# Kernel tuning notes

Measured on AMD Instinct MI355X. Metric: run time of the kernel, lower is better.

Reference implementation:

```python
import jax, jax.numpy as jnp
import numpy as np

HIDDEN = 4096
N_EXPERTS = 128
TOP_K = 8
N_GROUP = 1
TOPK_GROUP = 1
ROUTED_SCALING = 1.0
NORM_TOPK_PROB = True


def setup_inputs() -> dict:
    key = jax.random.key(0)
    k1, k2 = jax.random.split(key)
    tokens = 16384  # batch 4 * seq 4096
    hidden_states = jax.random.normal(k1, (tokens, HIDDEN), dtype=jnp.float32)
    # router gate weight (n_routed_experts, hidden_size)
    weight = jax.random.normal(k2, (N_EXPERTS, HIDDEN), dtype=jnp.float32) * 0.02
    # e_score_correction_bias buffer, initialized to zeros in the module
    e_score_correction_bias = jnp.zeros((N_EXPERTS,), dtype=jnp.float32)
    return {"hidden_states": hidden_states, "weight": weight,
            "e_score_correction_bias": e_score_correction_bias}


def _get_topk_indices(scores, bias):
    # scores: [T, E] sigmoid gate scores; bias: [E]
    T = scores.shape[0]
    experts_per_group = N_EXPERTS // N_GROUP
    s = scores + bias[None, :]  # scores_for_choice
    # group score: sum of top-2 corrected scores within each group
    grp = s.reshape(T, N_GROUP, experts_per_group)
    group_scores = jnp.sum(jax.lax.top_k(grp, 2)[0], axis=-1)  # [T, G]
    group_idx = jax.lax.top_k(group_scores, TOPK_GROUP)[1]      # [T, topk_group]
    group_mask = jnp.zeros((T, N_GROUP), dtype=bool).at[
        jnp.arange(T)[:, None], group_idx].set(True)
    score_mask = jnp.repeat(group_mask, experts_per_group, axis=-1)  # [T, E]
    s_masked = jnp.where(score_mask, s, 0.0)
    topk_indices = jax.lax.top_k(s_masked, TOP_K)[1]  # [T, top_k]
    return topk_indices


def reference(hidden_states, weight, e_score_correction_bias):
    x = hidden_states.reshape(-1, HIDDEN).astype(jnp.float32)
    router_logits = x @ weight.astype(jnp.float32).T          # [T, E]
    scores = jax.nn.sigmoid(router_logits)
    topk_indices = _get_topk_indices(scores, e_score_correction_bias)
    topk_weights = jnp.take_along_axis(scores, topk_indices, axis=1)  # [T, top_k]
    if NORM_TOPK_PROB:
        denom = jnp.sum(topk_weights, axis=-1, keepdims=True) + 1e-20
        topk_weights = topk_weights / denom
    topk_weights = topk_weights * ROUTED_SCALING
    return topk_indices, topk_weights
```

## Files before the change

### kernel.cpp

```cpp
#include <hip/hip_runtime.h>
#include <math.h>

#define HIDDEN 4096
#define NEXP   128
#define TOPK   8
#define BT     32
#define CHUNK  64
#define NCHUNK (HIDDEN / CHUNK)
#define SSTR   132
#define PLANE  (NEXP * CHUNK)

typedef int v4i __attribute__((ext_vector_type(4)));

static __device__ __forceinline__ unsigned pack4(int a, int b, int c, int d) {
    return (unsigned)(a & 255) | ((unsigned)(b & 255) << 8) |
           ((unsigned)(c & 255) << 16) | ((unsigned)(d & 255) << 24);
}

static __device__ __forceinline__ void slice5(float val, float scale1,
        int& d0, int& d1, int& d2, int& d3, int& d4) {
    float v = val * scale1;
    float f = __builtin_rintf(v);
    float r = v - f;
    int nh = (int)f;
    int nl = (int)__builtin_rintf(r * 2097152.0f);
    d0 = (nh + 64) >> 7;  d1 = nh - (d0 << 7);
    d2 = (nl + 8192) >> 14;
    int r2 = nl - (d2 << 14);
    d3 = (r2 + 64) >> 7;  d4 = r2 - (d3 << 7);
}

static __device__ __forceinline__ void slice4(float val, float scale1,
        int& d0, int& d1, int& d2, int& d3) {
    float v = val * scale1;
    float f = __builtin_rintf(v);
    float r = v - f;
    int nh = (int)f;
    int nl = (int)__builtin_rintf(r * 16384.0f);
    d0 = (nh + 64) >> 7;  d1 = nh - (d0 << 7);
    d2 = (nl + 64) >> 7;  d3 = nl - (d2 << 7);
}

__global__ __launch_bounds__(256)
void slice_w_kernel(const float* __restrict__ W, signed char* __restrict__ P)
{
    const int t  = blockIdx.x * 256 + threadIdx.x;
    const int e  = t >> 9;
    const int k0 = (t & 511) * 8;
    const float* src = W + (size_t)e * HIDDEN + k0;
    const float4 a = ((const float4*)src)[0];
    const float4 b = ((const float4*)src)[1];

    int p00,p01,p02,p03,p04; slice5(a.x, 32768.0f, p00,p01,p02,p03,p04);
    int p10,p11,p12,p13,p14; slice5(a.y, 32768.0f, p10,p11,p12,p13,p14);
    int p20,p21,p22,p23,p24; slice5(a.z, 32768.0f, p20,p21,p22,p23,p24);
    int p30,p31,p32,p33,p34; slice5(a.w, 32768.0f, p30,p31,p32,p33,p34);
    int p40,p41,p42,p43,p44; slice5(b.x, 32768.0f, p40,p41,p42,p43,p44);
    int p50,p51,p52,p53,p54; slice5(b.y, 32768.0f, p50,p51,p52,p53,p54);
    int p60,p61,p62,p63,p64; slice5(b.z, 32768.0f, p60,p61,p62,p63,p64);
    int p70,p71,p72,p73,p74; slice5(b.w, 32768.0f, p70,p71,p72,p73,p74);

    const int c = k0 >> 6, kin = k0 & 63;
    signed char* base = P + ((size_t)(c * 5) * NEXP + e) * CHUNK + kin;
    uint2 v;
    v.x = pack4(p00,p10,p20,p30); v.y = pack4(p40,p50,p60,p70);
    *(uint2*)(base + 0 * PLANE) = v;
    v.x = pack4(p01,p11,p21,p31); v.y = pack4(p41,p51,p61,p71);
    *(uint2*)(base + 1 * PLANE) = v;
    v.x = pack4(p02,p12,p22,p32); v.y = pack4(p42,p52,p62,p72);
    *(uint2*)(base + 2 * PLANE) = v;
    v.x = pack4(p03,p13,p23,p33); v.y = pack4(p43,p53,p63,p73);
    *(uint2*)(base + 3 * PLANE) = v;
    v.x = pack4(p04,p14,p24,p34); v.y = pack4(p44,p54,p64,p74);
    *(uint2*)(base + 4 * PLANE) = v;
}

static __device__ __forceinline__ void slice_pack16(
        const float4 f0, const float4 f1, const float4 f2, const float4 f3,
        v4i& s0, v4i& s1, v4i& s2, v4i& s3)
{
    unsigned w0[4], w1[4], w2[4], w3[4];
    {
        int a0,b0,c0,d0, a1,b1,c1,d1, a2,b2,c2,d2, a3,b3,c3,d3;
        slice4(f0.x, 1024.0f, a0,a1,a2,a3);
        slice4(f0.y, 1024.0f, b0,b1,b2,b3);
        slice4(f0.z, 1024.0f, c0,c1,c2,c3);
        slice4(f0.w, 1024.0f, d0,d1,d2,d3);
        w0[0] = pack4(a0,b0,c0,d0); w1[0] = pack4(a1,b1,c1,d1);
        w2[0] = pack4(a2,b2,c2,d2); w3[0] = pack4(a3,b3,c3,d3);
    }
    {
        int a0,b0,c0,d0, a1,b1,c1,d1, a2,b2,c2,d2, a3,b3,c3,d3;
        slice4(f1.x, 1024.0f, a0,a1,a2,a3);
        slice4(f1.y, 1024.0f, b0,b1,b2,b3);
        slice4(f1.z, 1024.0f, c0,c1,c2,c3);
        slice4(f1.w, 1024.0f, d0,d1,d2,d3);
        w0[1] = pack4(a0,b0,c0,d0); w1[1] = pack4(a1,b1,c1,d1);
        w2[1] = pack4(a2,b2,c2,d2); w3[1] = pack4(a3,b3,c3,d3);
    }
    {
        int a0,b0,c0,d0, a1,b1,c1,d1, a2,b2,c2,d2, a3,b3,c3,d3;
        slice4(f2.x, 1024.0f, a0,a1,a2,a3);
        slice4(f2.y, 1024.0f, b0,b1,b2,b3);
        slice4(f2.z, 1024.0f, c0,c1,c2,c3);
        slice4(f2.w, 1024.0f, d0,d1,d2,d3);
        w0[2] = pack4(a0,b0,c0,d0); w1[2] = pack4(a1,b1,c1,d1);
        w2[2] = pack4(a2,b2,c2,d2); w3[2] = pack4(a3,b3,c3,d3);
    }
    {
        int a0,b0,c0,d0, a1,b1,c1,d1, a2,b2,c2,d2, a3,b3,c3,d3;
        slice4(f3.x, 1024.0f, a0,a1,a2,a3);
        slice4(f3.y, 1024.0f, b0,b1,b2,b3);
        slice4(f3.z, 1024.0f, c0,c1,c2,c3);
        slice4(f3.w, 1024.0f, d0,d1,d2,d3);
        w0[3] = pack4(a0,b0,c0,d0); w1[3] = pack4(a1,b1,c1,d1);
        w2[3] = pack4(a2,b2,c2,d2); w3[3] = pack4(a3,b3,c3,d3);
    }
    s0 = (v4i){(int)w0[0], (int)w0[1], (int)w0[2], (int)w0[3]};
    s1 = (v4i){(int)w1[0], (int)w1[1], (int)w1[2], (int)w1[3]};
    s2 = (v4i){(int)w2[0], (int)w2[1], (int)w2[2], (int)w2[3]};
    s3 = (v4i){(int)w3[0], (int)w3[1], (int)w3[2], (int)w3[3]};
}

__global__ __launch_bounds__(256, 2)
void router_kernel(const float* __restrict__ X,
                   const signed char* __restrict__ P,
                   const float* __restrict__ Bias,
                   float* __restrict__ Out, int T)
{
    __shared__ double S[BT * SSTR];

    const int tid  = threadIdx.x;
    const int lane = tid & 63;
    const int wave = tid >> 6;
    const int tokBase = blockIdx.x * BT;

    const int m = lane & 15;
    const int q = lane >> 4;

    int r0 = tokBase + m;      if (r0 >= T) r0 = T - 1;
    int r1 = tokBase + 16 + m; if (r1 >= T) r1 = T - 1;
    const float* xp0 = X + (size_t)r0 * HIDDEN + q * 16;
    const float* xp1 = X + (size_t)r1 * HIDDEN + q * 16;

    const int eb0 = wave * 32 + m;
    const size_t boff0 = (size_t)eb0 * CHUNK + q * 16;
    const size_t boff1 = boff0 + (size_t)16 * CHUNK;

    v4i acc[2][2][5];
    #pragma unroll
    for (int tt = 0; tt < 2; tt++)
        #pragma unroll
        for (int et = 0; et < 2; et++)
            #pragma unroll
            for (int s = 0; s < 5; s++)
                acc[tt][et][s] = (v4i){0, 0, 0, 0};

    #pragma unroll 2
    for (int c = 0; c < NCHUNK; c++) {
        const float4* x0 = (const float4*)(xp0 + c * CHUNK);
        const float4* x1 = (const float4*)(xp1 + c * CHUNK);
        const float4 f00 = x0[0], f01 = x0[1], f02 = x0[2], f03 = x0[3];
        const float4 f10 = x1[0], f11 = x1[1], f12 = x1[2], f13 = x1[3];

        const signed char* pc = P + (size_t)(c * 5) * PLANE;
        v4i b0[5], b1[5];
        #pragma unroll
        for (int s = 0; s < 5; s++) {
            b0[s] = *(const v4i*)(pc + (size_t)s * PLANE + boff0);
            b1[s] = *(const v4i*)(pc + (size_t)s * PLANE + boff1);
        }

        v4i a0[4], a1[4];
        slice_pack16(f00, f01, f02, f03, a0[0], a0[1], a0[2], a0[3]);
        slice_pack16(f10, f11, f12, f13, a1[0], a1[1], a1[2], a1[3]);

        #pragma unroll
        for (int tt = 0; tt < 2; tt++) {
            const v4i A0 = tt ? a1[0] : a0[0];
            const v4i A1 = tt ? a1[1] : a0[1];
            const v4i A2 = tt ? a1[2] : a0[2];
            const v4i A3 = tt ? a1[3] : a0[3];
            #pragma unroll
            for (int et = 0; et < 2; et++) {
                const v4i B0 = et ? b1[0] : b0[0];
                const v4i B1 = et ? b1[1] : b0[1];
                const v4i B2 = et ? b1[2] : b0[2];
                const v4i B3 = et ? b1[3] : b0[3];
                const v4i B4 = et ? b1[4] : b0[4];
                acc[tt][et][0] = __builtin_amdgcn_mfma_i32_16x16x64_i8(A0, B0, acc[tt][et][0], 0, 0, 0);
                acc[tt][et][1] = __builtin_amdgcn_mfma_i32_16x16x64_i8(A0, B1, acc[tt][et][1], 0, 0, 0);
                acc[tt][et][1] = __builtin_amdgcn_mfma_i32_16x16x64_i8(A1, B0, acc[tt][et][1], 0, 0, 0);
                acc[tt][et][2] = __builtin_amdgcn_mfma_i32_16x16x64_i8(A0, B2, acc[tt][et][2], 0, 0, 0);
                acc[tt][et][2] = __builtin_amdgcn_mfma_i32_16x16x64_i8(A1, B1, acc[tt][et][2], 0, 0, 0);
                acc[tt][et][2] = __builtin_amdgcn_mfma_i32_16x16x64_i8(A2, B0, acc[tt][et][2], 0, 0, 0);
                acc[tt][et][3] = __builtin_amdgcn_mfma_i32_16x16x64_i8(A0, B3, acc[tt][et][3], 0, 0, 0);
                acc[tt][et][3] = __builtin_amdgcn_mfma_i32_16x16x64_i8(A1, B2, acc[tt][et][3], 0, 0, 0);
                acc[tt][et][3] = __builtin_amdgcn_mfma_i32_16x16x64_i8(A2, B1, acc[tt][et][3], 0, 0, 0);
                acc[tt][et][3] = __builtin_amdgcn_mfma_i32_16x16x64_i8(A3, B0, acc[tt][et][3], 0, 0, 0);
                acc[tt][et][4] = __builtin_amdgcn_mfma_i32_16x16x64_i8(A0, B4, acc[tt][et][4], 0, 0, 0);
                acc[tt][et][4] = __builtin_amdgcn_mfma_i32_16x16x64_i8(A1, B3, acc[tt][et][4], 0, 0, 0);
                acc[tt][et][4] = __builtin_amdgcn_mfma_i32_16x16x64_i8(A2, B2, acc[tt][et][4], 0, 0, 0);
                acc[tt][et][4] = __builtin_amdgcn_mfma_i32_16x16x64_i8(A3, B1, acc[tt][et][4], 0, 0, 0);
            }
        }
    }

    {
        const double w0 = 0x1p-11, w1 = 0x1p-18, w2 = 0x1p-25, w3 = 0x1p-32, w4 = 0x1p-39;
        #pragma unroll
        for (int tt = 0; tt < 2; tt++)
            #pragma unroll
            for (int et = 0; et < 2; et++) {
                const int ecol = wave * 32 + et * 16 + m;
                const double bias = (double)Bias[ecol];
                #pragma unroll
                for (int r = 0; r < 4; r++) {
                    const int trow = tt * 16 + q * 4 + r;
                    const double logit = (double)acc[tt][et][0][r] * w0
                                       + (double)acc[tt][et][1][r] * w1
                                       + (double)acc[tt][et][2][r] * w2
                                       + (double)acc[tt][et][3][r] * w3
                                       + (double)acc[tt][et][4][r] * w4;
                    S[trow * SSTR + ecol] = 1.0 / (1.0 + exp(-logit)) + bias;
                }
            }
    }
    __syncthreads();

    {
        const int tk  = tid >> 3;
        const int j   = tid & 7;
        const int tok = tokBase + tk;
        const double* row = S + tk * SSTR + j * 16;
        double v[16];
        #pragma unroll
        for (int k = 0; k < 16; k++) v[k] = row[k];

        double wts[TOPK]; float idxf[TOPK];
        double wsum = 0.0;
        #pragma unroll
        for (int p = 0; p < TOPK; p++) {
            double best = v[0]; int bi = 0;
            #pragma unroll
            for (int k = 1; k < 16; k++)
                if (v[k] > best) { best = v[k]; bi = k; }
            int be = j * 16 + bi;
            #pragma unroll
            for (int off = 1; off < 8; off <<= 1) {
                double ob = __shfl_xor(best, off, 8);
                int    oe = __shfl_xor(be,   off, 8);
                if (ob > best || (ob == best && oe < be)) { best = ob; be = oe; }
            }
            const bool own = (be >> 4) == j;
            const int  bl  = be & 15;
            #pragma unroll
            for (int k = 0; k < 16; k++)
                if (own && k == bl) v[k] = -1.0e300;
            const double sg = best - (double)Bias[be];
            wts[p]  = sg;
            wsum   += sg;
            idxf[p] = (float)be;
        }
        if (j == 0 && tok < T) {
            const double inv = 1.0 / (wsum + 1e-20);
            float* oi = Out + (size_t)tok * TOPK;
            float* ow = Out + (size_t)T * TOPK + (size_t)tok * TOPK;
            #pragma unroll
            for (int p = 0; p < TOPK; p++) {
                oi[p] = idxf[p];
                ow[p] = (float)(wts[p] * inv);
            }
        }
    }
}

extern "C" void kernel_launch(void* const* d_in, const int* in_sizes, int n_in,
                              void* d_out, int out_size, void* d_ws, size_t ws_size,
                              hipStream_t stream) {
    const float* X    = (const float*)d_in[0];
    const float* W    = (const float*)d_in[1];
    const float* Bias = (const float*)d_in[2];
    float* Out = (float*)d_out;
    const int T = in_sizes[0] / HIDDEN;
    signed char* P = (signed char*)d_ws;

    hipLaunchKernelGGL(slice_w_kernel, dim3(NEXP * 512 / 256), dim3(256), 0, stream, W, P);
    hipLaunchKernelGGL(router_kernel, dim3((T + BT - 1) / BT), dim3(256), 0, stream,
                       X, P, Bias, Out, T);
}
```

Measured before the change: 508.5 us.

## Double token tile per block, prefetch activations, drop lowest-order slice products

Each block now handles 64 tokens, with each wave covering 32 tokens by 64 experts, so every loaded weight fragment feeds more MFMAs. Activation loads are software-pipelined two chunks ahead, and slicing runs one chunk ahead of the MFMAs. The lowest-significance weight slice (plane 4) is no longer loaded or multiplied, which cuts MFMA and load work but reduces the precision of the emulated fp32 logits. Launch bounds move to one block per SM to make room for the larger accumulator set, and the top-k phase uses 4 threads per token instead of 8.

```diff
diff --git a/kernel.cpp b/kernel.cpp
--- a/kernel.cpp
+++ b/kernel.cpp
@@ -4,7 +4,7 @@
 #define HIDDEN 4096
 #define NEXP   128
 #define TOPK   8
-#define BT     32
+#define BT     64
 #define CHUNK  64
 #define NCHUNK (HIDDEN / CHUNK)
 #define SSTR   132
@@ -122,7 +122,7 @@
     s3 = (v4i){(int)w3[0], (int)w3[1], (int)w3[2], (int)w3[3]};
 }
 
-__global__ __launch_bounds__(256, 2)
+__global__ __launch_bounds__(256, 1)
 void router_kernel(const float* __restrict__ X,
                    const signed char* __restrict__ P,
                    const float* __restrict__ Bias,
@@ -137,57 +137,76 @@
 
     const int m = lane & 15;
     const int q = lane >> 4;
-
-    int r0 = tokBase + m;      if (r0 >= T) r0 = T - 1;
-    int r1 = tokBase + 16 + m; if (r1 >= T) r1 = T - 1;
+    const int tpair = wave & 1;
+    const int ehalf = wave >> 1;
+
+    int r0 = tokBase + tpair * 32 + m;      if (r0 >= T) r0 = T - 1;
+    int r1 = tokBase + tpair * 32 + 16 + m; if (r1 >= T) r1 = T - 1;
     const float* xp0 = X + (size_t)r0 * HIDDEN + q * 16;
     const float* xp1 = X + (size_t)r1 * HIDDEN + q * 16;
 
-    const int eb0 = wave * 32 + m;
-    const size_t boff0 = (size_t)eb0 * CHUNK + q * 16;
-    const size_t boff1 = boff0 + (size_t)16 * CHUNK;
-
-    v4i acc[2][2][5];
+    const size_t boffBase = (size_t)(ehalf * 64 + m) * CHUNK + (size_t)q * 16;
+
+    v4i acc[2][4][5];
     #pragma unroll
     for (int tt = 0; tt < 2; tt++)
         #pragma unroll
-        for (int et = 0; et < 2; et++)
+        for (int et = 0; et < 4; et++)
             #pragma unroll
             for (int s = 0; s < 5; s++)
                 acc[tt][et][s] = (v4i){0, 0, 0, 0};
 
-    #pragma unroll 2
+    v4i aC[2][4];
+    float4 xn[8];
+    {
+        const float4* x0 = (const float4*)xp0;
+        const float4* x1 = (const float4*)xp1;
+        const float4 c0 = x0[0], c1 = x0[1], c2 = x0[2], c3 = x0[3];
+        const float4 c4 = x1[0], c5 = x1[1], c6 = x1[2], c7 = x1[3];
+        slice_pack16(c0, c1, c2, c3, aC[0][0], aC[0][1], aC[0][2], aC[0][3]);
+        slice_pack16(c4, c5, c6, c7, aC[1][0], aC[1][1], aC[1][2], aC[1][3]);
+        const float4* y0 = (const float4*)(xp0 + CHUNK);
+        const float4* y1 = (const float4*)(xp1 + CHUNK);
+        xn[0] = y0[0]; xn[1] = y0[1]; xn[2] = y0[2]; xn[3] = y0[3];
+        xn[4] = y1[0]; xn[5] = y1[1]; xn[6] = y1[2]; xn[7] = y1[3];
+    }
+
+    #pragma unroll 1
     for (int c = 0; c < NCHUNK; c++) {
-        const float4* x0 = (const float4*)(xp0 + c * CHUNK);
-        const float4* x1 = (const float4*)(xp1 + c * CHUNK);
-        const float4 f00 = x0[0], f01 = x0[1], f02 = x0[2], f03 = x0[3];
-        const float4 f10 = x1[0], f11 = x1[1], f12 = x1[2], f13 = x1[3];
-
         const signed char* pc = P + (size_t)(c * 5) * PLANE;
-        v4i b0[5], b1[5];
-        #pragma unroll
-        for (int s = 0; s < 5; s++) {
-            b0[s] = *(const v4i*)(pc + (size_t)s * PLANE + boff0);
-            b1[s] = *(const v4i*)(pc + (size_t)s * PLANE + boff1);
+        v4i B[4][4];
+        #pragma unroll
+        for (int et = 0; et < 4; et++)
+            #pragma unroll
+            for (int s = 0; s < 4; s++)
+                B[et][s] = *(const v4i*)(pc + (size_t)s * PLANE + boffBase
+                                            + (size_t)(et * 16) * CHUNK);
+
+        float4 x2[8];
+        {
+            const int cn = (c + 2) & (NCHUNK - 1);
+            const float4* y0 = (const float4*)(xp0 + cn * CHUNK);
+            const float4* y1 = (const float4*)(xp1 + cn * CHUNK);
+            x2[0] = y0[0]; x2[1] = y0[1]; x2[2] = y0[2]; x2[3] = y0[3];
+            x2[4] = y1[0]; x2[5] = y1[1]; x2[6] = y1[2]; x2[7] = y1[3];
         }
 
-        v4i a0[4], a1[4];
-        slice_pack16(f00, f01, f02, f03, a0[0], a0[1], a0[2], a0[3]);
-        slice_pack16(f10, f11, f12, f13, a1[0], a1[1], a1[2], a1[3]);
+        v4i aN[2][4];
+        slice_pack16(xn[0], xn[1], xn[2], xn[3], aN[0][0], aN[0][1], aN[0][2], aN[0][3]);
+        slice_pack16(xn[4], xn[5], xn[6], xn[7], aN[1][0], aN[1][1], aN[1][2], aN[1][3]);
 
         #pragma unroll
         for (int tt = 0; tt < 2; tt++) {
-            const v4i A0 = tt ? a1[0] : a0[0];
-            const v4i A1 = tt ? a1[1] : a0[1];
-            const v4i A2 = tt ? a1[2] : a0[2];
-            const v4i A3 = tt ? a1[3] : a0[3];
-            #pragma unroll
-            for (int et = 0; et < 2; et++) {
-                const v4i B0 = et ? b1[0] : b0[0];
-                const v4i B1 = et ? b1[1] : b0[1];
-                const v4i B2 = et ? b1[2] : b0[2];
-                const v4i B3 = et ? b1[3] : b0[3];
-                const v4i B4 = et ? b1[4] : b0[4];
+            const v4i A0 = aC[tt][0];
+            const v4i A1 = aC[tt][1];
+            const v4i A2 = aC[tt][2];
+            const v4i A3 = aC[tt][3];
+            #pragma unroll
+            for (int et = 0; et < 4; et++) {
+                const v4i B0 = B[et][0];
+                const v4i B1 = B[et][1];
+                const v4i B2 = B[et][2];
+                const v4i B3 = B[et][3];
                 acc[tt][et][0] = __builtin_amdgcn_mfma_i32_16x16x64_i8(A0, B0, acc[tt][et][0], 0, 0, 0);
                 acc[tt][et][1] = __builtin_amdgcn_mfma_i32_16x16x64_i8(A0, B1, acc[tt][et][1], 0, 0, 0);
                 acc[tt][et][1] = __builtin_amdgcn_mfma_i32_16x16x64_i8(A1, B0, acc[tt][et][1], 0, 0, 0);
@@ -198,12 +217,20 @@
                 acc[tt][et][3] = __builtin_amdgcn_mfma_i32_16x16x64_i8(A1, B2, acc[tt][et][3], 0, 0, 0);
                 acc[tt][et][3] = __builtin_amdgcn_mfma_i32_16x16x64_i8(A2, B1, acc[tt][et][3], 0, 0, 0);
                 acc[tt][et][3] = __builtin_amdgcn_mfma_i32_16x16x64_i8(A3, B0, acc[tt][et][3], 0, 0, 0);
-                acc[tt][et][4] = __builtin_amdgcn_mfma_i32_16x16x64_i8(A0, B4, acc[tt][et][4], 0, 0, 0);
                 acc[tt][et][4] = __builtin_amdgcn_mfma_i32_16x16x64_i8(A1, B3, acc[tt][et][4], 0, 0, 0);
                 acc[tt][et][4] = __builtin_amdgcn_mfma_i32_16x16x64_i8(A2, B2, acc[tt][et][4], 0, 0, 0);
                 acc[tt][et][4] = __builtin_amdgcn_mfma_i32_16x16x64_i8(A3, B1, acc[tt][et][4], 0, 0, 0);
             }
         }
+
+        #pragma unroll
+        for (int i = 0; i < 2; i++)
+            #pragma unroll
+            for (int s = 0; s < 4; s++)
+                aC[i][s] = aN[i][s];
+        #pragma unroll
+        for (int i = 0; i < 8; i++)
+            xn[i] = x2[i];
     }
 
     {
@@ -211,12 +238,12 @@
         #pragma unroll
         for (int tt = 0; tt < 2; tt++)
             #pragma unroll
-            for (int et = 0; et < 2; et++) {
-                const int ecol = wave * 32 + et * 16 + m;
+            for (int et = 0; et < 4; et++) {
+                const int ecol = ehalf * 64 + et * 16 + m;
                 const double bias = (double)Bias[ecol];
                 #pragma unroll
                 for (int r = 0; r < 4; r++) {
-                    const int trow = tt * 16 + q * 4 + r;
+                    const int trow = tpair * 32 + tt * 16 + q * 4 + r;
                     const double logit = (double)acc[tt][et][0][r] * w0
                                        + (double)acc[tt][et][1][r] * w1
                                        + (double)acc[tt][et][2][r] * w2
@@ -229,13 +256,13 @@
     __syncthreads();
 
     {
-        const int tk  = tid >> 3;
-        const int j   = tid & 7;
+        const int tk  = tid >> 2;
+        const int j   = tid & 3;
         const int tok = tokBase + tk;
-        const double* row = S + tk * SSTR + j * 16;
-        double v[16];
-        #pragma unroll
-        for (int k = 0; k < 16; k++) v[k] = row[k];
+        const double* row = S + tk * SSTR + j * 32;
+        double v[32];
+        #pragma unroll
+        for (int k = 0; k < 32; k++) v[k] = row[k];
 
         double wts[TOPK]; float idxf[TOPK];
         double wsum = 0.0;
@@ -243,19 +270,19 @@
         for (int p = 0; p < TOPK; p++) {
             double best = v[0]; int bi = 0;
             #pragma unroll
-            for (int k = 1; k < 16; k++)
+            for (int k = 1; k < 32; k++)
                 if (v[k] > best) { best = v[k]; bi = k; }
-            int be = j * 16 + bi;
-            #pragma unroll
-            for (int off = 1; off < 8; off <<= 1) {
-                double ob = __shfl_xor(best, off, 8);
-                int    oe = __shfl_xor(be,   off, 8);
+            int be = j * 32 + bi;
+            #pragma unroll
+            for (int off = 1; off < 4; off <<= 1) {
+                double ob = __shfl_xor(best, off, 4);
+                int    oe = __shfl_xor(be,   off, 4);
                 if (ob > best || (ob == best && oe < be)) { best = ob; be = oe; }
             }
-            const bool own = (be >> 4) == j;
-            const int  bl  = be & 15;
-            #pragma unroll
-            for (int k = 0; k < 16; k++)
+            const bool own = (be >> 5) == j;
+            const int  bl  = be & 31;
+            #pragma unroll
+            for (int k = 0; k < 32; k++)
                 if (own && k == bl) v[k] = -1.0e300;
             const double sg = best - (double)Bias[be];
             wts[p]  = sg;
```

Result: slower. 685.1 us (+34.7%).

## Double-buffer chunk loads, widen block to 64 tokens, drop lowest slice product

Applied to the files above, without the earlier changes.

The router kernel becomes a software-pipelined loop: while the MFMAs for the current chunk run, the next chunk's X values and int8 weight slices are loaded into separate even and odd register buffers. Blocks grow to 512 threads and 64 tokens, and the waves are split across token halves and expert quarters. The sliced product now uses 13 MFMAs instead of 14 and loads 4 weight planes instead of 5, dropping the A0*B4 term. That removes work but slightly lowers logit precision, and the larger block uses more registers and LDS.

```diff
diff --git a/kernel.cpp b/kernel.cpp
--- a/kernel.cpp
+++ b/kernel.cpp
@@ -4,7 +4,7 @@
 #define HIDDEN 4096
 #define NEXP   128
 #define TOPK   8
-#define BT     32
+#define BT     64
 #define CHUNK  64
 #define NCHUNK (HIDDEN / CHUNK)
 #define SSTR   132
@@ -122,7 +122,22 @@
     s3 = (v4i){(int)w3[0], (int)w3[1], (int)w3[2], (int)w3[3]};
 }
 
-__global__ __launch_bounds__(256, 2)
+#define PYR13(A0, A1, A2, A3, BF, ACC)                                         \
+    ACC[0] = __builtin_amdgcn_mfma_i32_16x16x64_i8(A0, BF[0], ACC[0], 0, 0, 0); \
+    ACC[1] = __builtin_amdgcn_mfma_i32_16x16x64_i8(A0, BF[1], ACC[1], 0, 0, 0); \
+    ACC[2] = __builtin_amdgcn_mfma_i32_16x16x64_i8(A0, BF[2], ACC[2], 0, 0, 0); \
+    ACC[3] = __builtin_amdgcn_mfma_i32_16x16x64_i8(A0, BF[3], ACC[3], 0, 0, 0); \
+    ACC[4] = __builtin_amdgcn_mfma_i32_16x16x64_i8(A1, BF[3], ACC[4], 0, 0, 0); \
+    ACC[1] = __builtin_amdgcn_mfma_i32_16x16x64_i8(A1, BF[0], ACC[1], 0, 0, 0); \
+    ACC[2] = __builtin_amdgcn_mfma_i32_16x16x64_i8(A1, BF[1], ACC[2], 0, 0, 0); \
+    ACC[3] = __builtin_amdgcn_mfma_i32_16x16x64_i8(A1, BF[2], ACC[3], 0, 0, 0); \
+    ACC[4] = __builtin_amdgcn_mfma_i32_16x16x64_i8(A2, BF[2], ACC[4], 0, 0, 0); \
+    ACC[2] = __builtin_amdgcn_mfma_i32_16x16x64_i8(A2, BF[0], ACC[2], 0, 0, 0); \
+    ACC[3] = __builtin_amdgcn_mfma_i32_16x16x64_i8(A2, BF[1], ACC[3], 0, 0, 0); \
+    ACC[4] = __builtin_amdgcn_mfma_i32_16x16x64_i8(A3, BF[1], ACC[4], 0, 0, 0); \
+    ACC[3] = __builtin_amdgcn_mfma_i32_16x16x64_i8(A3, BF[0], ACC[3], 0, 0, 0);
+
+__global__ __launch_bounds__(512, 2)
 void router_kernel(const float* __restrict__ X,
                    const signed char* __restrict__ P,
                    const float* __restrict__ Bias,
@@ -135,16 +150,17 @@
     const int wave = tid >> 6;
     const int tokBase = blockIdx.x * BT;
 
-    const int m = lane & 15;
-    const int q = lane >> 4;
-
-    int r0 = tokBase + m;      if (r0 >= T) r0 = T - 1;
-    int r1 = tokBase + 16 + m; if (r1 >= T) r1 = T - 1;
+    const int m  = lane & 15;
+    const int q  = lane >> 4;
+    const int tp = wave & 1;
+    const int eq = wave >> 1;
+
+    int r0 = tokBase + tp * 32 + m;      if (r0 >= T) r0 = T - 1;
+    int r1 = tokBase + tp * 32 + 16 + m; if (r1 >= T) r1 = T - 1;
     const float* xp0 = X + (size_t)r0 * HIDDEN + q * 16;
     const float* xp1 = X + (size_t)r1 * HIDDEN + q * 16;
 
-    const int eb0 = wave * 32 + m;
-    const size_t boff0 = (size_t)eb0 * CHUNK + q * 16;
+    const size_t boff0 = (size_t)(eq * 32 + m) * CHUNK + (size_t)q * 16;
     const size_t boff1 = boff0 + (size_t)16 * CHUNK;
 
     v4i acc[2][2][5];
@@ -156,53 +172,64 @@
             for (int s = 0; s < 5; s++)
                 acc[tt][et][s] = (v4i){0, 0, 0, 0};
 
-    #pragma unroll 2
-    for (int c = 0; c < NCHUNK; c++) {
-        const float4* x0 = (const float4*)(xp0 + c * CHUNK);
-        const float4* x1 = (const float4*)(xp1 + c * CHUNK);
+    v4i bfE[2][4], bfO[2][4];
+    #pragma unroll
+    for (int s = 0; s < 4; s++) {
+        bfE[0][s] = *(const v4i*)(P + (size_t)s * PLANE + boff0);
+        bfE[1][s] = *(const v4i*)(P + (size_t)s * PLANE + boff1);
+    }
+    v4i aE0[4], aE1[4], aO0[4], aO1[4];
+    {
+        const float4* x0 = (const float4*)xp0;
+        const float4* x1 = (const float4*)xp1;
         const float4 f00 = x0[0], f01 = x0[1], f02 = x0[2], f03 = x0[3];
         const float4 f10 = x1[0], f11 = x1[1], f12 = x1[2], f13 = x1[3];
-
-        const signed char* pc = P + (size_t)(c * 5) * PLANE;
-        v4i b0[5], b1[5];
-        #pragma unroll
-        for (int s = 0; s < 5; s++) {
-            b0[s] = *(const v4i*)(pc + (size_t)s * PLANE + boff0);
-            b1[s] = *(const v4i*)(pc + (size_t)s * PLANE + boff1);
+        slice_pack16(f00, f01, f02, f03, aE0[0], aE0[1], aE0[2], aE0[3]);
+        slice_pack16(f10, f11, f12, f13, aE1[0], aE1[1], aE1[2], aE1[3]);
+    }
+
+    #pragma unroll 1
+    for (int c = 0; c < NCHUNK; c += 2) {
+        {
+            const signed char* pn = P + (size_t)((c + 1) * 5) * PLANE;
+            #pragma unroll
+            for (int s = 0; s < 4; s++) {
+                bfO[0][s] = *(const v4i*)(pn + (size_t)s * PLANE + boff0);
+                bfO[1][s] = *(const v4i*)(pn + (size_t)s * PLANE + boff1);
+            }
+            const float4* x0 = (const float4*)(xp0 + (c + 1) * CHUNK);
+            const float4* x1 = (const float4*)(xp1 + (c + 1) * CHUNK);
+            const float4 f00 = x0[0], f01 = x0[1], f02 = x0[2], f03 = x0[3];
+            const float4 f10 = x1[0], f11 = x1[1], f12 = x1[2], f13 = x1[3];
+
+            PYR13(aE0[0], aE0[1], aE0[2], aE0[3], bfE[0], acc[0][0])
+            PYR13(aE0[0], aE0[1], aE0[2], aE0[3], bfE[1], acc[0][1])
+            PYR13(aE1[0], aE1[1], aE1[2], aE1[3], bfE[0], acc[1][0])
+            PYR13(aE1[0], aE1[1], aE1[2], aE1[3], bfE[1], acc[1][1])
+
+            slice_pack16(f00, f01, f02, f03, aO0[0], aO0[1], aO0[2], aO0[3]);
+            slice_pack16(f10, f11, f12, f13, aO1[0], aO1[1], aO1[2], aO1[3]);
         }
-
-        v4i a0[4], a1[4];
-        slice_pack16(f00, f01, f02, f03, a0[0], a0[1], a0[2], a0[3]);
-        slice_pack16(f10, f11, f12, f13, a1[0], a1[1], a1[2], a1[3]);
-
-        #pragma unroll
-        for (int tt = 0; tt < 2; tt++) {
-            const v4i A0 = tt ? a1[0] : a0[0];
-            const v4i A1 = tt ? a1[1] : a0[1];
-            const v4i A2 = tt ? a1[2] : a0[2];
-            const v4i A3 = tt ? a1[3] : a0[3];
-            #pragma unroll
-            for (int et = 0; et < 2; et++) {
-                const v4i B0 = et ? b1[0] : b0[0];
-                const v4i B1 = et ? b1[1] : b0[1];
-                const v4i B2 = et ? b1[2] : b0[2];
-                const v4i B3 = et ? b1[3] : b0[3];
-                const v4i B4 = et ? b1[4] : b0[4];
-                acc[tt][et][0] = __builtin_amdgcn_mfma_i32_16x16x64_i8(A0, B0, acc[tt][et][0], 0, 0, 0);
-                acc[tt][et][1] = __builtin_amdgcn_mfma_i32_16x16x64_i8(A0, B1, acc[tt][et][1], 0, 0, 0);
-                acc[tt][et][1] = __builtin_amdgcn_mfma_i32_16x16x64_i8(A1, B0, acc[tt][et][1], 0, 0, 0);
-                acc[tt][et][2] = __builtin_amdgcn_mfma_i32_16x16x64_i8(A0, B2, acc[tt][et][2], 0, 0, 0);
-                acc[tt][et][2] = __builtin_amdgcn_mfma_i32_16x16x64_i8(A1, B1, acc[tt][et][2], 0, 0, 0);
-                acc[tt][et][2] = __builtin_amdgcn_mfma_i32_16x16x64_i8(A2, B0, acc[tt][et][2], 0, 0, 0);
-                acc[tt][et][3] = __builtin_amdgcn_mfma_i32_16x16x64_i8(A0, B3, acc[tt][et][3], 0, 0, 0);
-                acc[tt][et][3] = __builtin_amdgcn_mfma_i32_16x16x64_i8(A1, B2, acc[tt][et][3], 0, 0, 0);
-                acc[tt][et][3] = __builtin_amdgcn_mfma_i32_16x16x64_i8(A2, B1, acc[tt][et][3], 0, 0, 0);
-                acc[tt][et][3] = __builtin_amdgcn_mfma_i32_16x16x64_i8(A3, B0, acc[tt][et][3], 0, 0, 0);
-                acc[tt][et][4] = __builtin_amdgcn_mfma_i32_16x16x64_i8(A0, B4, acc[tt][et][4], 0, 0, 0);
-                acc[tt][et][4] = __builtin_amdgcn_mfma_i32_16x16x64_i8(A1, B3, acc[tt][et][4], 0, 0, 0);
-                acc[tt][et][4] = __builtin_amdgcn_mfma_i32_16x16x64_i8(A2, B2, acc[tt][et][4], 0, 0, 0);
-                acc[tt][et][4] = __builtin_amdgcn_mfma_i32_16x16x64_i8(A3, B1, acc[tt][et][4], 0, 0, 0);
-            }
+        {
+            const signed char* pn = P + (size_t)(((c + 2) & (NCHUNK - 1)) * 5) * PLANE;
+            #pragma unroll
+            for (int s = 0; s < 4; s++) {
+                bfE[0][s] = *(const v4i*)(pn + (size_t)s * PLANE + boff0);
+                bfE[1][s] = *(const v4i*)(pn + (size_t)s * PLANE + boff1);
+            }
+            const int cn = (c + 2) & (NCHUNK - 1);
+            const float4* x0 = (const float4*)(xp0 + cn * CHUNK);
+            const float4* x1 = (const float4*)(xp1 + cn * CHUNK);
+            const float4 f00 = x0[0], f01 = x0[1], f02 = x0[2], f03 = x0[3];
+            const float4 f10 = x1[0], f11 = x1[1], f12 = x1[2], f13 = x1[3];
+
+            PYR13(aO0[0], aO0[1], aO0[2], aO0[3], bfO[0], acc[0][0])
+            PYR13(aO0[0], aO0[1], aO0[2], aO0[3], bfO[1], acc[0][1])
+            PYR13(aO1[0], aO1[1], aO1[2], aO1[3], bfO[0], acc[1][0])
+            PYR13(aO1[0], aO1[1], aO1[2], aO1[3], bfO[1], acc[1][1])
+
+            slice_pack16(f00, f01, f02, f03, aE0[0], aE0[1], aE0[2], aE0[3]);
+            slice_pack16(f10, f11, f12, f13, aE1[0], aE1[1], aE1[2], aE1[3]);
         }
     }
 
@@ -212,11 +239,11 @@
         for (int tt = 0; tt < 2; tt++)
             #pragma unroll
             for (int et = 0; et < 2; et++) {
-                const int ecol = wave * 32 + et * 16 + m;
+                const int ecol = eq * 32 + et * 16 + m;
                 const double bias = (double)Bias[ecol];
                 #pragma unroll
                 for (int r = 0; r < 4; r++) {
-                    const int trow = tt * 16 + q * 4 + r;
+                    const int trow = tp * 32 + tt * 16 + q * 4 + r;
                     const double logit = (double)acc[tt][et][0][r] * w0
                                        + (double)acc[tt][et][1][r] * w1
                                        + (double)acc[tt][et][2][r] * w2
@@ -286,6 +313,6 @@
     signed char* P = (signed char*)d_ws;
 
     hipLaunchKernelGGL(slice_w_kernel, dim3(NEXP * 512 / 256), dim3(256), 0, stream, W, P);
-    hipLaunchKernelGGL(router_kernel, dim3((T + BT - 1) / BT), dim3(256), 0, stream,
+    hipLaunchKernelGGL(router_kernel, dim3((T + BT - 1) / BT), dim3(512), 0, stream,
                        X, P, Bias, Out, T);
 }
```

After: 558.4 us. 1.1x slower.
